# Kernel optimization log

Hardware: AMD Instinct MI355X
Metric: run time of the kernel (lower is better)

The kernel has to match this reference:

```python
import jax, jax.numpy as jnp
import numpy as np

N_EMBD = 1024
BLOCK_SIZE = 2048
ATTN_SPAN = 256
LN_EPS = 1e-5


def _band_mask(T, span, dtype):
    ones = jnp.ones((T, T), dtype=dtype)
    # tril(.,0) * (1 - tril(.,-span)) -> causal band of width `span`
    return jnp.tril(ones, 0) * (1.0 - jnp.tril(ones, -span))


def setup_inputs() -> dict:
    key = jax.random.key(0)
    k_x, k_w, k_b, k_lw = jax.random.split(key, 4)
    B, T, C = 4, BLOCK_SIZE, N_EMBD
    x = jax.random.normal(k_x, (B, T, C), dtype=jnp.float32)
    # qkv_net: Linear(C, 3C) with bias (torch default)
    lim = 1.0 / np.sqrt(C)
    W_qkv = jax.random.uniform(k_w, (C, 3 * C), minval=-lim, maxval=lim, dtype=jnp.float32)
    b_qkv = jax.random.uniform(k_b, (3 * C,), minval=-lim, maxval=lim, dtype=jnp.float32)
    ln_w = jnp.ones((C,), dtype=jnp.float32)
    ln_b = jnp.zeros((C,), dtype=jnp.float32)
    return {"x": x, "W_qkv": W_qkv, "b_qkv": b_qkv, "ln_w": ln_w, "ln_b": ln_b}


def _layer_norm(h, w, b):
    mu = jnp.mean(h, axis=-1, keepdims=True)
    var = jnp.var(h, axis=-1, keepdims=True)
    return (h - mu) * jax.lax.rsqrt(var + LN_EPS) * w + b


def reference(x, W_qkv, b_qkv, ln_w, ln_b):
    B, T, C = x.shape
    qkv = x @ W_qkv + b_qkv  # [B,T,3C]
    q, k, v = jnp.split(qkv, 3, axis=-1)
    scale = np.sqrt(C * ATTN_SPAN).astype(np.float32)
    scores = jnp.einsum('bid,bjd->bij', q, k) / scale  # [B,T,T]
    scores = scores * _band_mask(T, ATTN_SPAN, x.dtype)[None, :, :]
    out = jnp.einsum('bij,bjd->bid', scores, v)  # [B,T,C]
    return _layer_norm(out, ln_w, ln_b)
```

## Files before the change

### kernel.cpp

```cpp
#include <hip/hip_runtime.h>
#include <cstdint>
#include <cstddef>

#define N_EMBD 1024
#define T_SEQ  2048
#define NBATCH 4
#define SPAN   256
#define C3     3072

typedef float  floatx4 __attribute__((ext_vector_type(4)));
typedef __bf16 bf16x8  __attribute__((ext_vector_type(8)));

__device__ inline unsigned short f2bf(float f) {
    union { float f; unsigned u; } x; x.f = f;
    unsigned u = x.u;
    unsigned r = (u + 0x7fffu + ((u >> 16) & 1u)) >> 16;
    return (unsigned short)r;
}

typedef __attribute__((address_space(1))) const void GVOID;
typedef __attribute__((address_space(3))) void LVOID;
__device__ inline void gl2lds16(const void* g, void* l) {
    __builtin_amdgcn_global_load_lds((GVOID*)g, (LVOID*)l, 16, 0, 0);
}


__device__ inline void stage_half128(const unsigned short* g, size_t stride,
                                     unsigned short* lds, int lane, int wave) {
#pragma unroll
    for (int rnd = 0; rnd < 2; rnd++) {
        const int r = rnd * 64 + wave * 8 + (lane >> 3);
        const int chunk = (lane & 7) ^ (r & 7);
        gl2lds16(g + (size_t)r * stride + chunk * 8, &lds[(rnd * 64 + wave * 8) * 64]);
    }
}

__device__ inline void stage_half64(const unsigned short* g, size_t stride,
                                    unsigned short* lds, int lane, int wave) {
    const int r = wave * 8 + (lane >> 3);
    const int chunk = (lane & 7) ^ (r & 7);
    gl2lds16(g + (size_t)r * stride + chunk * 8, &lds[(wave * 8) * 64]);
}

__device__ inline void stage64x64(const unsigned short* g, size_t stride,
                                  unsigned short* lds, int lane, int wave) {
#pragma unroll
    for (int rnd = 0; rnd < 2; rnd++) {
        const int r = rnd * 32 + wave * 8 + (lane >> 3);
        const int chunk = (lane & 7) ^ (r & 7);
        gl2lds16(g + (size_t)r * stride + chunk * 8, &lds[(rnd * 32 + wave * 8) * 64]);
    }
}

__device__ inline void stage128x64(const unsigned short* g, size_t stride,
                                   unsigned short* lds, int lane, int wave) {
#pragma unroll
    for (int rnd = 0; rnd < 4; rnd++) {
        const int r = rnd * 32 + wave * 8 + (lane >> 3);
        const int chunk = (lane & 7) ^ (r & 7);
        gl2lds16(g + (size_t)r * stride + chunk * 8, &lds[(rnd * 32 + wave * 8) * 64]);
    }
}

__device__ inline bf16x8 frag_ld(const unsigned short* buf, int row, int ks, int q) {
    return *(const bf16x8*)&buf[row * 64 + (((ks * 4 + q) ^ (row & 7)) * 8)];
}

__global__ __launch_bounds__(256) void k_prep(const float* __restrict__ x,
                                              unsigned short* __restrict__ Xb,
                                              const float* __restrict__ W,
                                              unsigned short* __restrict__ WbT) {
    __shared__ unsigned short t[32][33];
    if (blockIdx.x < 8192) {
        int i = (blockIdx.x * 256 + threadIdx.x) * 4;
        float4 v = *(const float4*)(x + i);
        ushort4 o;
        o.x = f2bf(v.x); o.y = f2bf(v.y); o.z = f2bf(v.z); o.w = f2bf(v.w);
        *(ushort4*)(Xb + i) = o;
    } else {
        int bid = blockIdx.x - 8192;
        int k0 = (bid & 31) * 32, n0 = (bid >> 5) * 32;
        int tx = threadIdx.x & 31, ty = threadIdx.x >> 5;
#pragma unroll
        for (int i = 0; i < 4; i++) {
            int k = k0 + ty + i * 8;
            t[ty + i * 8][tx] = f2bf(W[(size_t)k * C3 + n0 + tx]);
        }
        __syncthreads();
#pragma unroll
        for (int i = 0; i < 4; i++) {
            int n = n0 + ty + i * 8;
            WbT[(size_t)n * N_EMBD + k0 + tx] = t[tx][ty + i * 8];
        }
    }
}

__global__ __launch_bounds__(512) void k_gemm(const unsigned short* __restrict__ Xb,
                                              const unsigned short* __restrict__ WbT,
                                              const float* __restrict__ bqkv,
                                              unsigned short* __restrict__ QK,
                                              unsigned short* __restrict__ Vt) {
    __shared__ unsigned short As[2][256 * 64];
    __shared__ unsigned short Bs[2][128 * 64];
    const int tid = threadIdx.x, lane = tid & 63, wave = tid >> 6;
    const int wm = wave >> 2, wn = wave & 3;
    const int n15 = lane & 15, q = lane >> 4;

    const int wg = (blockIdx.x & 7) * 96 + (blockIdx.x >> 3);
    const bool isV = (wg >= 512);

    const unsigned short* gA;
    const unsigned short* gB;
    int rowbase, colbase, nb;
    if (!isV) {
        const int mt = wg >> 4, nt = wg & 15;
        gA = Xb + (size_t)(mt * 256) * N_EMBD;
        gB = WbT + (size_t)(nt * 128) * N_EMBD;
        rowbase = mt * 256; colbase = nt * 128; nb = nt * 128;
    } else {
        const int v = wg - 512;
        const int ct = v >> 6, tv = v & 63;
        const int t0 = tv * 128;
        gA = WbT + (size_t)(2048 + ct * 256) * N_EMBD;
        gB = Xb + (size_t)t0 * N_EMBD;
        rowbase = (t0 >> 11) * 1024 + ct * 256;
        colbase = t0 & 2047;
        nb = 2048 + ct * 256;
    }

    floatx4 acc[8][2] = {};

#define BAR __builtin_amdgcn_s_barrier()
#define MFMA8(MIBASE, NI)                                                          \
    __builtin_amdgcn_sched_barrier(0);                                             \
    __builtin_amdgcn_s_setprio(1);                                                 \
    _Pragma("unroll")                                                              \
    for (int ks = 0; ks < 2; ++ks)                                                 \
        _Pragma("unroll")                                                          \
        for (int mi = 0; mi < 4; ++mi)                                             \
            acc[(MIBASE) + mi][NI] = __builtin_amdgcn_mfma_f32_16x16x32_bf16(      \
                a[mi][ks], b[NI][ks], acc[(MIBASE) + mi][NI], 0, 0, 0);            \
    __builtin_amdgcn_s_setprio(0);                                                 \
    __builtin_amdgcn_sched_barrier(0);

    stage_half128(gA,                    N_EMBD, As[0],            lane, wave);
    stage_half128(gA + 128 * N_EMBD,     N_EMBD, As[0] + 128 * 64, lane, wave);
    stage_half64 (gB,                    N_EMBD, Bs[0],            lane, wave);
    stage_half64 (gB + 64 * N_EMBD,      N_EMBD, Bs[0] + 64 * 64,  lane, wave);
    stage_half64 (gB + 64,               N_EMBD, Bs[1],            lane, wave);
    stage_half64 (gB + 64 + 64 * N_EMBD, N_EMBD, Bs[1] + 64 * 64,  lane, wave);
    asm volatile("s_waitcnt vmcnt(2)" ::: "memory");
    BAR;

#pragma unroll 1
    for (int it = 0; it < 8; ++it) {
        const int t0k = it * 128;
        const int t1k = t0k + 64;
        const bool last = (it == 7);
        bf16x8 a[4][2], b[2][2];

#pragma unroll
        for (int mi = 0; mi < 4; ++mi)
#pragma unroll
            for (int ks = 0; ks < 2; ++ks)
                a[mi][ks] = frag_ld(As[0], wm * 128 + mi * 16 + n15, ks, q);
#pragma unroll
        for (int ks = 0; ks < 2; ++ks)
            b[0][ks] = frag_ld(Bs[0], wn * 32 + n15, ks, q);
        stage_half128(gA + t1k, N_EMBD, As[1], lane, wave);
        BAR;
        MFMA8(0, 0)
        BAR;
#pragma unroll
        for (int ks = 0; ks < 2; ++ks)
            b[1][ks] = frag_ld(Bs[0], wn * 32 + 16 + n15, ks, q);
        stage_half128(gA + t1k + 128 * N_EMBD, N_EMBD, As[1] + 128 * 64, lane, wave);
        BAR;
        MFMA8(0, 1)
        BAR;
#pragma unroll
        for (int mi = 0; mi < 4; ++mi)
#pragma unroll
            for (int ks = 0; ks < 2; ++ks)
                a[mi][ks] = frag_ld(As[0], wm * 128 + (mi + 4) * 16 + n15, ks, q);
        if (!last) stage_half64(gB + t0k + 128, N_EMBD, Bs[0], lane, wave);
        BAR;
        MFMA8(4, 1)
        BAR;
        if (!last) stage_half64(gB + t0k + 128 + 64 * N_EMBD, N_EMBD, Bs[0] + 64 * 64, lane, wave);
        BAR;
        MFMA8(4, 0)
        if (last) { asm volatile("s_waitcnt vmcnt(0)" ::: "memory"); }
        else      { asm volatile("s_waitcnt vmcnt(2)" ::: "memory"); }
        BAR;

#pragma unroll
        for (int mi = 0; mi < 4; ++mi)
#pragma unroll
            for (int ks = 0; ks < 2; ++ks)
                a[mi][ks] = frag_ld(As[1], wm * 128 + mi * 16 + n15, ks, q);
#pragma unroll
        for (int ks = 0; ks < 2; ++ks)
            b[0][ks] = frag_ld(Bs[1], wn * 32 + n15, ks, q);
        if (!last) stage_half128(gA + t0k + 128, N_EMBD, As[0], lane, wave);
        BAR;
        MFMA8(0, 0)
        BAR;
#pragma unroll
        for (int ks = 0; ks < 2; ++ks)
            b[1][ks] = frag_ld(Bs[1], wn * 32 + 16 + n15, ks, q);
        if (!last) stage_half128(gA + t0k + 128 + 128 * N_EMBD, N_EMBD, As[0] + 128 * 64, lane, wave);
        BAR;
        MFMA8(0, 1)
        BAR;
#pragma unroll
        for (int mi = 0; mi < 4; ++mi)
#pragma unroll
            for (int ks = 0; ks < 2; ++ks)
                a[mi][ks] = frag_ld(As[1], wm * 128 + (mi + 4) * 16 + n15, ks, q);
        if (!last) stage_half64(gB + t1k + 128, N_EMBD, Bs[1], lane, wave);
        BAR;
        MFMA8(4, 1)
        BAR;
        if (!last) stage_half64(gB + t1k + 128 + 64 * N_EMBD, N_EMBD, Bs[1] + 64 * 64, lane, wave);
        BAR;
        MFMA8(4, 0)
        if (!last) { asm volatile("s_waitcnt vmcnt(2)" ::: "memory"); }
        BAR;
    }
#undef MFMA8
#undef BAR

    unsigned short* base = isV ? Vt : QK;
#pragma unroll
    for (int mi = 0; mi < 8; ++mi) {
#pragma unroll
        for (int r = 0; r < 4; ++r) {
            const int arow = wm * 128 + mi * 16 + q * 4 + r;
            unsigned short* dst = base + (size_t)(rowbase + arow) * 2048 + colbase;
            const float rbias = bqkv[nb + arow];
#pragma unroll
            for (int ni = 0; ni < 2; ++ni) {
                const int acol = wn * 32 + ni * 16 + n15;
                const float bias = isV ? rbias : bqkv[nb + acol];
                dst[acol] = f2bf(acc[mi][ni][r] + bias);
            }
        }
    }
}

__global__ __launch_bounds__(256) void k_scores(const unsigned short* __restrict__ QK,
                                                unsigned short* __restrict__ S) {
    const int jj = blockIdx.x, qb = blockIdx.y, b = blockIdx.z;
    const int jb = qb - 4 + jj;
    if (jb < 0) return;

    __shared__ unsigned short Qs[4096];
    __shared__ unsigned short Ks[4096];
    const int tid = threadIdx.x, lane = tid & 63, wave = tid >> 6;
    const int wr = wave >> 1, wc = wave & 1;
    const int n15 = lane & 15, q = lane >> 4;

    floatx4 acc[2][2] = {};

    const unsigned short* gQ = QK + ((size_t)(b * T_SEQ + qb * 64)) * 2048;
    const unsigned short* gK = QK + ((size_t)(b * T_SEQ + jb * 64)) * 2048 + 1024;

    for (int k0 = 0; k0 < N_EMBD; k0 += 64) {
        stage64x64(gQ + k0, 2048, Qs, lane, wave);
        stage64x64(gK + k0, 2048, Ks, lane, wave);
        __syncthreads();
#pragma unroll
        for (int s = 0; s < 2; s++) {
            bf16x8 a[2], bbf[2];
#pragma unroll
            for (int mi = 0; mi < 2; mi++) {
                const int row = wr * 32 + mi * 16 + n15;
                a[mi] = *(const bf16x8*)&Qs[row * 64 + (((s * 4 + q) ^ (row & 7)) * 8)];
            }
#pragma unroll
            for (int ni = 0; ni < 2; ni++) {
                const int row = wc * 32 + ni * 16 + n15;
                bbf[ni] = *(const bf16x8*)&Ks[row * 64 + (((s * 4 + q) ^ (row & 7)) * 8)];
            }
#pragma unroll
            for (int mi = 0; mi < 2; mi++)
#pragma unroll
                for (int ni = 0; ni < 2; ni++)
                    acc[mi][ni] = __builtin_amdgcn_mfma_f32_16x16x32_bf16(a[mi], bbf[ni], acc[mi][ni], 0, 0, 0);
        }
        __syncthreads();
    }

    unsigned short* Sb = S + (((size_t)(b * 32 + qb) * 5 + jj) << 12);
#pragma unroll
    for (int mi = 0; mi < 2; mi++)
#pragma unroll
        for (int ni = 0; ni < 2; ni++)
#pragma unroll
            for (int r = 0; r < 4; r++) {
                const int il = wr * 32 + mi * 16 + q * 4 + r;
                const int jl = wc * 32 + ni * 16 + n15;
                const int gi = qb * 64 + il, gj = jb * 64 + jl;
                const float v = ((gj <= gi) && (gj > gi - SPAN)) ? acc[mi][ni][r] * (1.0f / 512.0f) : 0.0f;
                Sb[il * 64 + jl] = f2bf(v);
            }
}

__global__ __launch_bounds__(256) void k_sv(const unsigned short* __restrict__ S,
                                            const unsigned short* __restrict__ Vt,
                                            float* __restrict__ out) {
    const int cg = blockIdx.x, qb = blockIdx.y, b = blockIdx.z;
    const int c0 = cg * 128;

    __shared__ unsigned short Ss[4096];
    __shared__ unsigned short Vs[8192];
    const int tid = threadIdx.x, lane = tid & 63, wave = tid >> 6;
    const int wr = wave >> 1, wc = wave & 1;
    const int n15 = lane & 15, q = lane >> 4;

    floatx4 acc[2][4] = {};

    for (int jj = 0; jj < 5; jj++) {
        const int jb = qb - 4 + jj;
        if (jb < 0) continue;
        stage64x64(S + (((size_t)(b * 32 + qb) * 5 + jj) << 12), 64, Ss, lane, wave);
        stage128x64(Vt + ((size_t)(b * 1024 + c0)) * 2048 + jb * 64, 2048, Vs, lane, wave);
        __syncthreads();
#pragma unroll
        for (int s = 0; s < 2; s++) {
            bf16x8 a[2], bbf[4];
#pragma unroll
            for (int mi = 0; mi < 2; mi++) {
                const int row = wr * 32 + mi * 16 + n15;
                a[mi] = *(const bf16x8*)&Ss[row * 64 + (((s * 4 + q) ^ (row & 7)) * 8)];
            }
#pragma unroll
            for (int ni = 0; ni < 4; ni++) {
                const int row = wc * 64 + ni * 16 + n15;
                bbf[ni] = *(const bf16x8*)&Vs[row * 64 + (((s * 4 + q) ^ (row & 7)) * 8)];
            }
#pragma unroll
            for (int mi = 0; mi < 2; mi++)
#pragma unroll
                for (int ni = 0; ni < 4; ni++)
                    acc[mi][ni] = __builtin_amdgcn_mfma_f32_16x16x32_bf16(a[mi], bbf[ni], acc[mi][ni], 0, 0, 0);
        }
        __syncthreads();
    }

#pragma unroll
    for (int mi = 0; mi < 2; mi++)
#pragma unroll
        for (int ni = 0; ni < 4; ni++)
#pragma unroll
            for (int r = 0; r < 4; r++) {
                const int il = wr * 32 + mi * 16 + q * 4 + r;
                const int cl = wc * 64 + ni * 16 + n15;
                out[((size_t)(b * T_SEQ + qb * 64 + il)) * N_EMBD + c0 + cl] = acc[mi][ni][r];
            }
}

__global__ __launch_bounds__(256) void k_ln(float* __restrict__ out,
                                            const float* __restrict__ w,
                                            const float* __restrict__ bias) {
    __shared__ float red[8];
    const int t = threadIdx.x;
    float* p = out + (size_t)blockIdx.x * N_EMBD;
    float4 v = ((const float4*)p)[t];
    float s  = v.x + v.y + v.z + v.w;
    float sq = v.x * v.x + v.y * v.y + v.z * v.z + v.w * v.w;
#pragma unroll
    for (int off = 32; off; off >>= 1) {
        s  += __shfl_down(s, off, 64);
        sq += __shfl_down(sq, off, 64);
    }
    const int wave = t >> 6, lane = t & 63;
    if (lane == 0) { red[wave] = s; red[4 + wave] = sq; }
    __syncthreads();
    const float ts = red[0] + red[1] + red[2] + red[3];
    const float tq = red[4] + red[5] + red[6] + red[7];
    const float mean = ts * (1.0f / N_EMBD);
    const float var  = tq * (1.0f / N_EMBD) - mean * mean;
    const float rs = rsqrtf(var + 1e-5f);
    float4 wv = ((const float4*)w)[t];
    float4 bv = ((const float4*)bias)[t];
    float4 o;
    o.x = (v.x - mean) * rs * wv.x + bv.x;
    o.y = (v.y - mean) * rs * wv.y + bv.y;
    o.z = (v.z - mean) * rs * wv.z + bv.z;
    o.w = (v.w - mean) * rs * wv.w + bv.w;
    ((float4*)p)[t] = o;
}

extern "C" void kernel_launch(void* const* d_in, const int* in_sizes, int n_in,
                              void* d_out, int out_size, void* d_ws, size_t ws_size,
                              hipStream_t stream) {
    const float* x  = (const float*)d_in[0];
    const float* W  = (const float*)d_in[1];
    const float* bq = (const float*)d_in[2];
    const float* lw = (const float*)d_in[3];
    const float* lb = (const float*)d_in[4];
    float* out = (float*)d_out;
    char* ws = (char*)d_ws;

    unsigned short* Xb   = (unsigned short*)(ws + 0);
    unsigned short* Sbuf = (unsigned short*)(ws + 0);
    unsigned short* WbT  = (unsigned short*)(ws + 16777216);
    unsigned short* QK   = (unsigned short*)(ws + 23068672);
    unsigned short* Vt   = (unsigned short*)(ws + 56623104);

    k_prep   <<<11264,           256, 0, stream>>>(x, Xb, W, WbT);
    k_gemm   <<<768,             512, 0, stream>>>(Xb, WbT, bq, QK, Vt);
    k_scores <<<dim3(5, 32, 4),  256, 0, stream>>>(QK, Sbuf);
    k_sv     <<<dim3(8, 32, 4),  256, 0, stream>>>(Sbuf, Vt, out);
    k_ln     <<<8192,            256, 0, stream>>>(out, lw, lb);
}
```

Before: 235.1 us.

## Restructure QKV GEMM main loop into two 16-MFMA phases with fused staging

Result: faster. 219.0 us (-6.8%).

```diff
diff --git a/kernel.cpp b/kernel.cpp
--- a/kernel.cpp
+++ b/kernel.cpp
@@ -33,13 +33,6 @@
         const int chunk = (lane & 7) ^ (r & 7);
         gl2lds16(g + (size_t)r * stride + chunk * 8, &lds[(rnd * 64 + wave * 8) * 64]);
     }
-}
-
-__device__ inline void stage_half64(const unsigned short* g, size_t stride,
-                                    unsigned short* lds, int lane, int wave) {
-    const int r = wave * 8 + (lane >> 3);
-    const int chunk = (lane & 7) ^ (r & 7);
-    gl2lds16(g + (size_t)r * stride + chunk * 8, &lds[(wave * 8) * 64]);
 }
 
 __device__ inline void stage64x64(const unsigned short* g, size_t stride,
@@ -131,25 +124,24 @@
     floatx4 acc[8][2] = {};
 
 #define BAR __builtin_amdgcn_s_barrier()
-#define MFMA8(MIBASE, NI)                                                          \
-    __builtin_amdgcn_sched_barrier(0);                                             \
+#define MFMA16(MIBASE)                                                             \
     __builtin_amdgcn_s_setprio(1);                                                 \
     _Pragma("unroll")                                                              \
     for (int ks = 0; ks < 2; ++ks)                                                 \
         _Pragma("unroll")                                                          \
         for (int mi = 0; mi < 4; ++mi)                                             \
-            acc[(MIBASE) + mi][NI] = __builtin_amdgcn_mfma_f32_16x16x32_bf16(      \
-                a[mi][ks], b[NI][ks], acc[(MIBASE) + mi][NI], 0, 0, 0);            \
-    __builtin_amdgcn_s_setprio(0);                                                 \
-    __builtin_amdgcn_sched_barrier(0);
-
-    stage_half128(gA,                    N_EMBD, As[0],            lane, wave);
-    stage_half128(gA + 128 * N_EMBD,     N_EMBD, As[0] + 128 * 64, lane, wave);
-    stage_half64 (gB,                    N_EMBD, Bs[0],            lane, wave);
-    stage_half64 (gB + 64 * N_EMBD,      N_EMBD, Bs[0] + 64 * 64,  lane, wave);
-    stage_half64 (gB + 64,               N_EMBD, Bs[1],            lane, wave);
-    stage_half64 (gB + 64 + 64 * N_EMBD, N_EMBD, Bs[1] + 64 * 64,  lane, wave);
-    asm volatile("s_waitcnt vmcnt(2)" ::: "memory");
+            _Pragma("unroll")                                                      \
+            for (int ni = 0; ni < 2; ++ni)                                         \
+                acc[(MIBASE) + mi][ni] = __builtin_amdgcn_mfma_f32_16x16x32_bf16(  \
+                    a[mi][ks], b[ni][ks], acc[(MIBASE) + mi][ni], 0, 0, 0);        \
+    __builtin_amdgcn_s_setprio(0);
+
+    stage_half128(gA,                N_EMBD, As[0],            lane, wave);
+    stage_half128(gA + 128 * N_EMBD, N_EMBD, As[0] + 128 * 64, lane, wave);
+    stage_half128(gB,                N_EMBD, Bs[0],            lane, wave);
+    stage_half128(gA + 64,           N_EMBD, As[1],            lane, wave);
+    stage_half128(gB + 64,           N_EMBD, Bs[1],            lane, wave);
+    asm volatile("s_waitcnt vmcnt(4)" ::: "memory");
     BAR;
 
 #pragma unroll 1
@@ -165,33 +157,28 @@
             for (int ks = 0; ks < 2; ++ks)
                 a[mi][ks] = frag_ld(As[0], wm * 128 + mi * 16 + n15, ks, q);
 #pragma unroll
-        for (int ks = 0; ks < 2; ++ks)
-            b[0][ks] = frag_ld(Bs[0], wn * 32 + n15, ks, q);
-        stage_half128(gA + t1k, N_EMBD, As[1], lane, wave);
-        BAR;
-        MFMA8(0, 0)
-        BAR;
-#pragma unroll
-        for (int ks = 0; ks < 2; ++ks)
-            b[1][ks] = frag_ld(Bs[0], wn * 32 + 16 + n15, ks, q);
+        for (int ni = 0; ni < 2; ++ni)
+#pragma unroll
+            for (int ks = 0; ks < 2; ++ks)
+                b[ni][ks] = frag_ld(Bs[0], wn * 32 + ni * 16 + n15, ks, q);
         stage_half128(gA + t1k + 128 * N_EMBD, N_EMBD, As[1] + 128 * 64, lane, wave);
         BAR;
-        MFMA8(0, 1)
-        BAR;
+        MFMA16(0)
+        BAR;
+
 #pragma unroll
         for (int mi = 0; mi < 4; ++mi)
 #pragma unroll
             for (int ks = 0; ks < 2; ++ks)
                 a[mi][ks] = frag_ld(As[0], wm * 128 + (mi + 4) * 16 + n15, ks, q);
-        if (!last) stage_half64(gB + t0k + 128, N_EMBD, Bs[0], lane, wave);
-        BAR;
-        MFMA8(4, 1)
-        BAR;
-        if (!last) stage_half64(gB + t0k + 128 + 64 * N_EMBD, N_EMBD, Bs[0] + 64 * 64, lane, wave);
-        BAR;
-        MFMA8(4, 0)
+        if (!last) {
+            stage_half128(gA + t0k + 128, N_EMBD, As[0], lane, wave);
+            stage_half128(gB + t0k + 128, N_EMBD, Bs[0], lane, wave);
+        }
+        BAR;
+        MFMA16(4)
         if (last) { asm volatile("s_waitcnt vmcnt(0)" ::: "memory"); }
-        else      { asm volatile("s_waitcnt vmcnt(2)" ::: "memory"); }
+        else      { asm volatile("s_waitcnt vmcnt(4)" ::: "memory"); }
         BAR;
 
 #pragma unroll
@@ -200,35 +187,30 @@
             for (int ks = 0; ks < 2; ++ks)
                 a[mi][ks] = frag_ld(As[1], wm * 128 + mi * 16 + n15, ks, q);
 #pragma unroll
-        for (int ks = 0; ks < 2; ++ks)
-            b[0][ks] = frag_ld(Bs[1], wn * 32 + n15, ks, q);
-        if (!last) stage_half128(gA + t0k + 128, N_EMBD, As[0], lane, wave);
-        BAR;
-        MFMA8(0, 0)
-        BAR;
-#pragma unroll
-        for (int ks = 0; ks < 2; ++ks)
-            b[1][ks] = frag_ld(Bs[1], wn * 32 + 16 + n15, ks, q);
+        for (int ni = 0; ni < 2; ++ni)
+#pragma unroll
+            for (int ks = 0; ks < 2; ++ks)
+                b[ni][ks] = frag_ld(Bs[1], wn * 32 + ni * 16 + n15, ks, q);
         if (!last) stage_half128(gA + t0k + 128 + 128 * N_EMBD, N_EMBD, As[0] + 128 * 64, lane, wave);
         BAR;
-        MFMA8(0, 1)
-        BAR;
+        MFMA16(0)
+        BAR;
+
 #pragma unroll
         for (int mi = 0; mi < 4; ++mi)
 #pragma unroll
             for (int ks = 0; ks < 2; ++ks)
                 a[mi][ks] = frag_ld(As[1], wm * 128 + (mi + 4) * 16 + n15, ks, q);
-        if (!last) stage_half64(gB + t1k + 128, N_EMBD, Bs[1], lane, wave);
-        BAR;
-        MFMA8(4, 1)
-        BAR;
-        if (!last) stage_half64(gB + t1k + 128 + 64 * N_EMBD, N_EMBD, Bs[1] + 64 * 64, lane, wave);
-        BAR;
-        MFMA8(4, 0)
-        if (!last) { asm volatile("s_waitcnt vmcnt(2)" ::: "memory"); }
-        BAR;
-    }
-#undef MFMA8
+        if (!last) {
+            stage_half128(gA + t1k + 128, N_EMBD, As[1], lane, wave);
+            stage_half128(gB + t1k + 128, N_EMBD, Bs[1], lane, wave);
+        }
+        BAR;
+        MFMA16(4)
+        if (!last) { asm volatile("s_waitcnt vmcnt(4)" ::: "memory"); }
+        BAR;
+    }
+#undef MFMA16
 #undef BAR
 
     unsigned short* base = isV ? Vt : QK;
```
